# Performance work log

Measured on AMD Instinct MI355X. Metric: run time of the kernel, lower is better.

Reference implementation:

```python
import jax, jax.numpy as jnp
from jax import lax
import numpy as np

EPS = 1e-5  # BatchNorm eps


def setup_inputs() -> dict:
    key = jax.random.key(0)
    ks = jax.random.split(key, 4)
    T, B, C = 256, 128, 1024
    L, H, NCLS = 6, 1024, 1000
    x = jax.random.normal(ks[0], (T, B, C), dtype=jnp.float32)
    W = jax.random.normal(ks[1], (L, C, H), dtype=jnp.float32) * (1.0 / np.sqrt(C))
    b = jnp.zeros((L, H), dtype=jnp.float32)
    gamma = jnp.ones((L, H), dtype=jnp.float32)
    beta = jnp.zeros((L, H), dtype=jnp.float32)
    u = jax.random.uniform(ks[2], (L, H), dtype=jnp.float32)  # recurrent weights in (0, U_bound~1)
    Wc = jax.random.normal(ks[3], (H, NCLS), dtype=jnp.float32) * (1.0 / np.sqrt(H))
    bc = jnp.zeros((NCLS,), dtype=jnp.float32)
    return {"x": x, "W": W, "b": b, "gamma": gamma, "beta": beta, "u": u, "Wc": Wc, "bc": bc}


def _layer(h, Wl, bl, gl, betal, ul):
    # per-timestep dense projection: [T,B,Cin] @ [Cin,H]
    z = jnp.einsum('tbi,ih->tbh', h, Wl) + bl
    # BN over (time, batch) per channel (bn_before, training-mode batch stats)
    mean = jnp.mean(z, axis=(0, 1))
    var = jnp.var(z, axis=(0, 1))
    z = (z - mean) * (gl / jnp.sqrt(var + EPS)) + betal
    # IndRNN diagonal recurrence: h_t = relu(z_t + u * h_{t-1}), h_0 = 0
    T, B, H = z.shape
    def step(hprev, zt):
        hnew = jax.nn.relu(zt + ul * hprev)
        return hnew, hnew
    _, hs = lax.scan(step, jnp.zeros((B, H), dtype=z.dtype), z)
    return hs


def reference(x, W, b, gamma, beta, u, Wc, bc):
    h = x
    for l in range(W.shape[0]):
        h = _layer(h, W[l], b[l], gamma[l], beta[l], u[l])
    # classifier on last timestep
    return h[-1] @ Wc + bc
```

## Files before the change

kernel.cpp:

```cpp
#include <hip/hip_runtime.h>
#include <hip/hip_bf16.h>

#define T_DIM 256
#define B_DIM 128
#define C_DIM 1024
#define H_DIM 1024
#define L_DIM 6
#define NC_DIM 1000
#define M_DIM (T_DIM * B_DIM)
#define BH_DIM (B_DIM * H_DIM)

typedef __attribute__((ext_vector_type(8))) short bf16x8;
typedef __attribute__((ext_vector_type(4))) float f32x4;

__device__ __forceinline__ float bf2f(unsigned short u) {
  union { unsigned int i; float f; } v; v.i = ((unsigned int)u) << 16; return v.f;
}
__device__ __forceinline__ unsigned short f2bf(float f) {
  union { float f; unsigned int i; } v; v.f = f;
  unsigned int r = v.i + 0x7fffu + ((v.i >> 16) & 1u);
  return (unsigned short)(r >> 16);
}

__device__ __forceinline__ void gload_lds16(const void* g, void* l) {
  __builtin_amdgcn_global_load_lds(
      (const __attribute__((address_space(1))) unsigned int*)g,
      (__attribute__((address_space(3))) unsigned int*)l, 16, 0, 0);
}

__global__ __launch_bounds__(256) void f32_to_bf16_kernel(
    const float* __restrict__ in, unsigned short* __restrict__ out, int n4) {
  int stride = gridDim.x * blockDim.x;
  for (int i = blockIdx.x * blockDim.x + threadIdx.x; i < n4; i += stride) {
    float4 v = ((const float4*)in)[i];
    ushort4 o;
    o.x = f2bf(v.x); o.y = f2bf(v.y); o.z = f2bf(v.z); o.w = f2bf(v.w);
    ((ushort4*)out)[i] = o;
  }
}

__global__ __launch_bounds__(256) void wtrans_kernel(
    const float* __restrict__ W, unsigned short* __restrict__ Wt) {
  __shared__ float tile[32][33];
  int l = blockIdx.z;
  const float* Wl = W + (size_t)l * C_DIM * H_DIM;
  unsigned short* Wtl = Wt + (size_t)l * C_DIM * H_DIM;
  int h0 = blockIdx.x * 32, c0 = blockIdx.y * 32;
  int tx = threadIdx.x, ty = threadIdx.y;
#pragma unroll
  for (int i = 0; i < 32; i += 8)
    tile[ty + i][tx] = Wl[(size_t)(c0 + ty + i) * H_DIM + h0 + tx];
  __syncthreads();
#pragma unroll
  for (int i = 0; i < 32; i += 8)
    Wtl[(size_t)(h0 + ty + i) * C_DIM + c0 + tx] = f2bf(tile[tx][ty + i]);
}

#define NT 16

__global__ __launch_bounds__(512, 2) void gemm_kernel(
    const unsigned short* __restrict__ A, const unsigned short* __restrict__ Bt,
    unsigned short* __restrict__ Z, float* __restrict__ psum, float* __restrict__ psqs) {
  extern __shared__ char lds[];
  int bid = blockIdx.x;
  int swz = (bid & 7) * 64 + (bid >> 3);
  int tm = swz >> 2, tn = swz & 3;
  int tid = threadIdx.x;
  int wv = tid >> 6, ln = tid & 63;
  int wm = wv >> 2, wn = wv & 3;

  const char* Apanel = (const char*)A + (size_t)tm * 256 * 2048;
  const char* Bpanel = (const char*)Bt + (size_t)tn * 256 * 2048;

  int srow0 = wv * 16 + (ln >> 2);
  int skey = (ln >> 3) & 3;
  int sclog = (ln & 3) ^ skey;
  size_t soff0 = (size_t)srow0 * 2048 + sclog * 16;
  size_t soff1 = (size_t)(128 + srow0) * 2048 + sclog * 16;
  int sdst = wv * 1024;

  auto stage = [&](int t, int region) {
    char* base = lds + ((t & 1) * 65536) + region * 16384;
    const char* src = (region < 2) ? Apanel : Bpanel;
    int kb = t * 128 + (region & 1) * 64;
    gload_lds16(src + soff0 + kb, base + sdst);
    gload_lds16(src + soff1 + kb, base + 8192 + sdst);
  };

  int frow = ln & 15;
  int fchunk = ((ln >> 4) ^ (frow >> 1)) & 3;
  int floff = frow * 64 + (fchunk << 4);

  f32x4 acc[8][4];
  f32x4 zero = {0.f, 0.f, 0.f, 0.f};
#pragma unroll
  for (int m = 0; m < 8; ++m)
#pragma unroll
    for (int n = 0; n < 4; ++n) acc[m][n] = zero;

  bf16x8 bfr[4], af[4];
  auto readB = [&](int t, int kk) {
    const char* Bb = lds + ((t & 1) * 65536) + 32768 + kk * 16384 + wn * 4096;
#pragma unroll
    for (int n = 0; n < 4; ++n) bfr[n] = *(const bf16x8*)(Bb + n * 1024 + floff);
  };
  auto readA = [&](int t, int kk, int mq) {
    const char* Ab = lds + ((t & 1) * 65536) + kk * 16384 + wm * 8192 + mq * 4096;
#pragma unroll
    for (int i = 0; i < 4; ++i) af[i] = *(const bf16x8*)(Ab + i * 1024 + floff);
  };
  auto mfma16 = [&](int mq) {
    __builtin_amdgcn_s_setprio(1);
#pragma unroll
    for (int i = 0; i < 4; ++i)
#pragma unroll
      for (int n = 0; n < 4; ++n)
        acc[mq * 4 + i][n] =
            __builtin_amdgcn_mfma_f32_16x16x32_bf16(af[i], bfr[n], acc[mq * 4 + i][n], 0, 0, 0);
    __builtin_amdgcn_s_setprio(0);
  };

  stage(0, 2); stage(0, 0); stage(0, 3); stage(0, 1);
  asm volatile("s_waitcnt vmcnt(4)" ::: "memory");
  __builtin_amdgcn_s_barrier();

  for (int t = 0; t < NT; ++t) {
    bool st = (t + 1 < NT);
    readB(t, 0); readA(t, 0, 0);
    if (st) stage(t + 1, 2);
    asm volatile("s_waitcnt lgkmcnt(0)" ::: "memory");
    __builtin_amdgcn_sched_barrier(0);
    mfma16(0);
    readA(t, 0, 1);
    if (st) stage(t + 1, 0);
    asm volatile("s_waitcnt lgkmcnt(0)" ::: "memory");
    __builtin_amdgcn_sched_barrier(0);
    mfma16(1);
    asm volatile("s_waitcnt vmcnt(4)" ::: "memory");
    __builtin_amdgcn_s_barrier();
    readB(t, 1); readA(t, 1, 0);
    if (st) stage(t + 1, 3);
    asm volatile("s_waitcnt lgkmcnt(0)" ::: "memory");
    __builtin_amdgcn_sched_barrier(0);
    mfma16(0);
    readA(t, 1, 1);
    if (st) stage(t + 1, 1);
    asm volatile("s_waitcnt lgkmcnt(0)" ::: "memory");
    __builtin_amdgcn_sched_barrier(0);
    mfma16(1);
    asm volatile("s_waitcnt vmcnt(4)" ::: "memory");
    __builtin_amdgcn_s_barrier();
  }

  float s[4], q[4];
#pragma unroll
  for (int n = 0; n < 4; ++n) {
    float sv = 0.f, qv = 0.f;
#pragma unroll
    for (int m = 0; m < 8; ++m)
#pragma unroll
      for (int r = 0; r < 4; ++r) {
        float v = acc[m][n][r];
        sv += v; qv += v * v;
      }
    s[n] = sv; q[n] = qv;
  }
#pragma unroll
  for (int n = 0; n < 4; ++n) {
    s[n] += __shfl_xor(s[n], 16); s[n] += __shfl_xor(s[n], 32);
    q[n] += __shfl_xor(q[n], 16); q[n] += __shfl_xor(q[n], 32);
  }
  float* red = (float*)lds;
  if (ln < 16) {
#pragma unroll
    for (int n = 0; n < 4; ++n) {
      red[wm * 256 + wn * 64 + n * 16 + ln] = s[n];
      red[512 + wm * 256 + wn * 64 + n * 16 + ln] = q[n];
    }
  }
  __syncthreads();
  if (tid < 256) {
    psum[(size_t)tm * H_DIM + tn * 256 + tid] = red[tid] + red[256 + tid];
  } else {
    int c = tid - 256;
    psqs[(size_t)tm * H_DIM + tn * 256 + c] = red[512 + c] + red[768 + c];
  }
  int r0 = tm * 256 + wm * 128 + ((ln >> 4) << 2);
  int c0 = tn * 256 + wn * 64 + (ln & 15);
#pragma unroll
  for (int m = 0; m < 8; ++m)
#pragma unroll
    for (int n = 0; n < 4; ++n) {
      unsigned short* zp = Z + (size_t)(r0 + m * 16) * H_DIM + c0 + n * 16;
#pragma unroll
      for (int r = 0; r < 4; ++r) zp[(size_t)r * H_DIM] = f2bf(acc[m][n][r]);
    }
}

__global__ __launch_bounds__(256) void bn_finalize_kernel(
    const float* __restrict__ psum, const float* __restrict__ psqs,
    const float* __restrict__ gamma, const float* __restrict__ beta,
    float* __restrict__ ss) {
  int c = blockIdx.x * blockDim.x + threadIdx.x;
  float s = 0.f, q = 0.f;
  for (int i = 0; i < 128; ++i) {
    s += psum[(size_t)i * H_DIM + c];
    q += psqs[(size_t)i * H_DIM + c];
  }
  const float invN = 1.0f / (float)M_DIM;
  float mean = s * invN;
  float var = q * invN - mean * mean;
  float sc = gamma[c] * rsqrtf(var + 1e-5f);
  ss[c] = sc;
  ss[H_DIM + c] = beta[c] - mean * sc;
}

__global__ __launch_bounds__(256) void bn_recur_kernel(
    const unsigned short* __restrict__ Z, const float* __restrict__ ss,
    const float* __restrict__ u, unsigned short* __restrict__ Hout) {
  int i = blockIdx.x * 256 + threadIdx.x;
  int h = i & (H_DIM - 1);
  float sc = ss[h], sh = ss[H_DIM + h], uu = u[h];
  float hv = 0.f;
  const unsigned short* Zt = Z + i;
  unsigned short* Ht = Hout + i;

  unsigned short za[32], zb[32];
#pragma unroll
  for (int j = 0; j < 32; ++j) za[j] = Zt[(size_t)j * BH_DIM];

#pragma unroll
  for (int blk = 0; blk < 4; ++blk) {
    int tA = blk * 64;
#pragma unroll
    for (int j = 0; j < 32; ++j) zb[j] = Zt[(size_t)(tA + 32 + j) * BH_DIM];
#pragma unroll
    for (int j = 0; j < 32; ++j) {
      float z = fmaf(bf2f(za[j]), sc, sh);
      hv = fmaxf(fmaf(uu, hv, z), 0.f);
      Ht[(size_t)(tA + j) * BH_DIM] = f2bf(hv);
    }
    if (blk < 3) {
#pragma unroll
      for (int j = 0; j < 32; ++j) za[j] = Zt[(size_t)(tA + 64 + j) * BH_DIM];
    }
#pragma unroll
    for (int j = 0; j < 32; ++j) {
      float z = fmaf(bf2f(zb[j]), sc, sh);
      hv = fmaxf(fmaf(uu, hv, z), 0.f);
      Ht[(size_t)(tA + 32 + j) * BH_DIM] = f2bf(hv);
    }
  }
}

__global__ __launch_bounds__(256) void classifier_kernel(
    const unsigned short* __restrict__ hlast, const float* __restrict__ Wc,
    const float* __restrict__ bc, float* __restrict__ out) {
  __shared__ float hs[H_DIM];
  int b = blockIdx.y;
  int n = blockIdx.x * 256 + threadIdx.x;
  for (int k = threadIdx.x; k < H_DIM; k += 256)
    hs[k] = bf2f(hlast[(size_t)b * H_DIM + k]);
  __syncthreads();
  if (n < NC_DIM) {
    float acc = bc[n];
#pragma unroll 8
    for (int k = 0; k < H_DIM; ++k)
      acc = fmaf(hs[k], Wc[(size_t)k * NC_DIM + n], acc);
    out[(size_t)b * NC_DIM + n] = acc;
  }
}

extern "C" void kernel_launch(void* const* d_in, const int* in_sizes, int n_in,
                              void* d_out, int out_size, void* d_ws, size_t ws_size,
                              hipStream_t stream) {
  const float* x     = (const float*)d_in[0];
  const float* W     = (const float*)d_in[1];
  const float* gamma = (const float*)d_in[3];
  const float* beta  = (const float*)d_in[4];
  const float* u     = (const float*)d_in[5];
  const float* Wc    = (const float*)d_in[6];
  const float* bc    = (const float*)d_in[7];
  float* out = (float*)d_out;

  const size_t CH = (size_t)C_DIM * H_DIM;
  const size_t MH = (size_t)M_DIM * H_DIM;
  char* p = (char*)d_ws;
  unsigned short* Wt = (unsigned short*)p; p += L_DIM * CH * sizeof(unsigned short);
  unsigned short* Ha = (unsigned short*)p; p += MH * sizeof(unsigned short);
  unsigned short* Hb = (unsigned short*)p; p += MH * sizeof(unsigned short);
  unsigned short* Z  = (unsigned short*)p; p += MH * sizeof(unsigned short);
  float* psum = (float*)p; p += 128 * H_DIM * sizeof(float);
  float* psqs = (float*)p; p += 128 * H_DIM * sizeof(float);
  float* ss   = (float*)p; p += 2 * H_DIM * sizeof(float);

  f32_to_bf16_kernel<<<2048, 256, 0, stream>>>(x, Ha, (int)(MH / 4));
  wtrans_kernel<<<dim3(H_DIM / 32, C_DIM / 32, L_DIM), dim3(32, 8), 0, stream>>>(W, Wt);

  unsigned short* cur = Ha;
  unsigned short* nxt = Hb;
  for (int l = 0; l < L_DIM; ++l) {
    gemm_kernel<<<(M_DIM / 256) * (H_DIM / 256), 512, 131072, stream>>>(
        cur, Wt + (size_t)l * CH, Z, psum, psqs);
    bn_finalize_kernel<<<4, 256, 0, stream>>>(psum, psqs, gamma + (size_t)l * H_DIM,
                                              beta + (size_t)l * H_DIM, ss);
    bn_recur_kernel<<<BH_DIM / 256, 256, 0, stream>>>(Z, ss, u + (size_t)l * H_DIM, nxt);
    unsigned short* tmp = cur; cur = nxt; nxt = tmp;
  }
  classifier_kernel<<<dim3(4, B_DIM), 256, 0, stream>>>(
      cur + (size_t)(T_DIM - 1) * BH_DIM, Wc, bc, out);
}
```

Baseline: 755.5 us.

## Restructure GEMM main loop into 4-deep LDS ring with register-prefetched fragments

```diff
diff --git a/kernel.cpp b/kernel.cpp
--- a/kernel.cpp
+++ b/kernel.cpp
@@ -56,7 +56,7 @@
     Wtl[(size_t)(h0 + ty + i) * C_DIM + c0 + tx] = f2bf(tile[tx][ty + i]);
 }
 
-#define NT 16
+#define NT 32
 
 __global__ __launch_bounds__(512, 2) void gemm_kernel(
     const unsigned short* __restrict__ A, const unsigned short* __restrict__ Bt,
@@ -72,19 +72,19 @@
   const char* Apanel = (const char*)A + (size_t)tm * 256 * 2048;
   const char* Bpanel = (const char*)Bt + (size_t)tn * 256 * 2048;
 
-  int srow0 = wv * 16 + (ln >> 2);
-  int skey = (ln >> 3) & 3;
-  int sclog = (ln & 3) ^ skey;
-  size_t soff0 = (size_t)srow0 * 2048 + sclog * 16;
-  size_t soff1 = (size_t)(128 + srow0) * 2048 + sclog * 16;
+  int p0 = wv * 1024 + ln * 16;
+  int l0 = p0 ^ (((p0 >> 7) & 3) << 4);
+  size_t ro0 = (size_t)(p0 >> 6) * 2048 + (l0 & 63);
+  size_t ro1 = (size_t)(128 + (p0 >> 6)) * 2048 + (l0 & 63);
   int sdst = wv * 1024;
 
-  auto stage = [&](int t, int region) {
-    char* base = lds + ((t & 1) * 65536) + region * 16384;
-    const char* src = (region < 2) ? Apanel : Bpanel;
-    int kb = t * 128 + (region & 1) * 64;
-    gload_lds16(src + soff0 + kb, base + sdst);
-    gload_lds16(src + soff1 + kb, base + 8192 + sdst);
+  auto stage = [&](int t) {
+    char* base = lds + ((t & 3) * 32768);
+    int kb = t * 64;
+    gload_lds16(Apanel + ro0 + kb, base + sdst);
+    gload_lds16(Apanel + ro1 + kb, base + 8192 + sdst);
+    gload_lds16(Bpanel + ro0 + kb, base + 16384 + sdst);
+    gload_lds16(Bpanel + ro1 + kb, base + 16384 + 8192 + sdst);
   };
 
   int frow = ln & 15;
@@ -98,58 +98,46 @@
 #pragma unroll
     for (int n = 0; n < 4; ++n) acc[m][n] = zero;
 
-  bf16x8 bfr[4], af[4];
-  auto readB = [&](int t, int kk) {
-    const char* Bb = lds + ((t & 1) * 65536) + 32768 + kk * 16384 + wn * 4096;
-#pragma unroll
-    for (int n = 0; n < 4; ++n) bfr[n] = *(const bf16x8*)(Bb + n * 1024 + floff);
+  bf16x8 bX[4], aP[4], aQ[4];
+  auto readB_to = [&](int t, bf16x8* d) {
+    const char* Bb = lds + ((t & 3) * 32768) + 16384 + wn * 4096;
+#pragma unroll
+    for (int n = 0; n < 4; ++n) d[n] = *(const bf16x8*)(Bb + n * 1024 + floff);
   };
-  auto readA = [&](int t, int kk, int mq) {
-    const char* Ab = lds + ((t & 1) * 65536) + kk * 16384 + wm * 8192 + mq * 4096;
-#pragma unroll
-    for (int i = 0; i < 4; ++i) af[i] = *(const bf16x8*)(Ab + i * 1024 + floff);
+  auto readA_to = [&](int t, int mq, bf16x8* d) {
+    const char* Ab = lds + ((t & 3) * 32768) + wm * 8192 + mq * 4096;
+#pragma unroll
+    for (int i = 0; i < 4; ++i) d[i] = *(const bf16x8*)(Ab + i * 1024 + floff);
   };
-  auto mfma16 = [&](int mq) {
-    __builtin_amdgcn_s_setprio(1);
-#pragma unroll
-    for (int i = 0; i < 4; ++i)
-#pragma unroll
-      for (int n = 0; n < 4; ++n)
-        acc[mq * 4 + i][n] =
-            __builtin_amdgcn_mfma_f32_16x16x32_bf16(af[i], bfr[n], acc[mq * 4 + i][n], 0, 0, 0);
-    __builtin_amdgcn_s_setprio(0);
-  };
-
-  stage(0, 2); stage(0, 0); stage(0, 3); stage(0, 1);
+
+  stage(0); stage(1); stage(2);
   asm volatile("s_waitcnt vmcnt(4)" ::: "memory");
   __builtin_amdgcn_s_barrier();
+  readB_to(0, bX); readA_to(0, 0, aP);
 
   for (int t = 0; t < NT; ++t) {
-    bool st = (t + 1 < NT);
-    readB(t, 0); readA(t, 0, 0);
-    if (st) stage(t + 1, 2);
-    asm volatile("s_waitcnt lgkmcnt(0)" ::: "memory");
-    __builtin_amdgcn_sched_barrier(0);
-    mfma16(0);
-    readA(t, 0, 1);
-    if (st) stage(t + 1, 0);
-    asm volatile("s_waitcnt lgkmcnt(0)" ::: "memory");
-    __builtin_amdgcn_sched_barrier(0);
-    mfma16(1);
-    asm volatile("s_waitcnt vmcnt(4)" ::: "memory");
-    __builtin_amdgcn_s_barrier();
-    readB(t, 1); readA(t, 1, 0);
-    if (st) stage(t + 1, 3);
-    asm volatile("s_waitcnt lgkmcnt(0)" ::: "memory");
-    __builtin_amdgcn_sched_barrier(0);
-    mfma16(0);
-    readA(t, 1, 1);
-    if (st) stage(t + 1, 1);
-    asm volatile("s_waitcnt lgkmcnt(0)" ::: "memory");
-    __builtin_amdgcn_sched_barrier(0);
-    mfma16(1);
-    asm volatile("s_waitcnt vmcnt(4)" ::: "memory");
-    __builtin_amdgcn_s_barrier();
+    readA_to(t, 1, aQ);
+    if (t <= NT - 4) stage(t + 3);
+    __builtin_amdgcn_s_setprio(1);
+#pragma unroll
+    for (int i = 0; i < 4; ++i)
+#pragma unroll
+      for (int n = 0; n < 4; ++n)
+        acc[i][n] = __builtin_amdgcn_mfma_f32_16x16x32_bf16(aP[i], bX[n], acc[i][n], 0, 0, 0);
+    __builtin_amdgcn_s_setprio(0);
+    __builtin_amdgcn_s_setprio(1);
+#pragma unroll
+    for (int i = 0; i < 4; ++i)
+#pragma unroll
+      for (int n = 0; n < 4; ++n)
+        acc[4 + i][n] = __builtin_amdgcn_mfma_f32_16x16x32_bf16(aQ[i], bX[n], acc[4 + i][n], 0, 0, 0);
+    __builtin_amdgcn_s_setprio(0);
+    if (t < NT - 1) {
+      readB_to(t + 1, bX); readA_to(t + 1, 0, aP);
+      if (t <= NT - 4) { asm volatile("s_waitcnt vmcnt(4)" ::: "memory"); }
+      else             { asm volatile("s_waitcnt vmcnt(0)" ::: "memory"); }
+      __builtin_amdgcn_s_barrier();
+    }
   }
 
   float s[4], q[4];
```

Measured after the change: 753.0 us. No clear change (-0.3%).
